# Optimization experiments

Measured on AMD Instinct MI355X. Metric: run time of the kernel, lower is better.

Reference implementation:

```python
import jax, jax.numpy as jnp
import numpy as np

B, N, C, CP, H, NQ, NK = 1, 2048, 128, 16, 8, 32, 128
DH = C // H
PAD = NK // 2 - NQ // 2  # 48
NB = N // NQ  # 64 windows


def _ln(x, gamma=None, beta=None, eps=1e-5):
    mu = jnp.mean(x, axis=-1, keepdims=True)
    var = jnp.var(x, axis=-1, keepdims=True)
    y = (x - mu) * jax.lax.rsqrt(var + eps)
    if gamma is not None:
        y = y * gamma
    if beta is not None:
        y = y + beta
    return y


def _forward(atom_single_repr, atom_single_proj, atom_pair_repr,
             gamma_s, Wg_ada, bg_ada, W_skip,
             gamma_p, beta_p, W_pair,
             Wq, Wk, Wv, Wg, bg, Wo, bo, W_out, b_out):
    # --- AdaLN(a, s): LN(a) modulated by s ---
    a_ln = _ln(atom_single_repr)                       # no affine
    s_ln = _ln(atom_single_proj, gamma_s)              # scale only
    a = jax.nn.sigmoid(s_ln @ Wg_ada + bg_ada) * a_ln + s_ln @ W_skip  # (B,N,C)

    # --- pair bias: LN + no-bias linear to heads ---
    pair_bias = _ln(atom_pair_repr, gamma_p, beta_p) @ W_pair          # (B,N,N,H)

    # --- extract_local_biases: pad key dim with -10000, take sliding blocks ---
    pb = jnp.pad(pair_bias, ((0, 0), (0, 0), (PAD, PAD), (0, 0)),
                 constant_values=-10000.0)                              # (B,N,N+2P,H)
    rows = pb.reshape(B, NB, NQ, N + 2 * PAD, H)
    col_idx = (jnp.arange(NB) * NQ)[:, None] + jnp.arange(NK)[None, :]  # (NB,NK)
    local_bias = jnp.take_along_axis(rows, col_idx[None, :, None, :, None], axis=3)
    bias = jnp.transpose(local_bias, (0, 1, 4, 2, 3))                   # (B,NB,H,NQ,NK)

    # --- partition_tensor for queries (stride==size, no pad) and keys/values ---
    q_x = a.reshape(B, NB, NQ, C)
    a_pad = jnp.pad(a, ((0, 0), (PAD, PAD), (0, 0)))
    kv_x = a_pad[:, col_idx, :]                                         # (B,NB,NK,C)

    # --- OpenFold-style gated attention per window ---
    q = (q_x @ Wq).reshape(B, NB, NQ, H, DH) * (DH ** -0.5)
    k = (kv_x @ Wk).reshape(B, NB, NK, H, DH)
    v = (kv_x @ Wv).reshape(B, NB, NK, H, DH)
    logits = jnp.einsum('bwqhd,bwkhd->bwhqk', q, k) + bias
    attn = jax.nn.softmax(logits, axis=-1)
    o = jnp.einsum('bwhqk,bwkhd->bwqhd', attn, v).reshape(B, NB, NQ, C)
    g = jax.nn.sigmoid(q_x @ Wg + bg)
    o = (o * g) @ Wo + bo                                               # (B,NB,NQ,C)
    out = o.reshape(B, N, C)

    # --- output gating ---
    return jax.nn.sigmoid(out @ W_out + b_out) * out


def setup_inputs() -> dict:
    key = jax.random.key(0)
    ks = jax.random.split(key, 16)
    s = 0.02
    return {
        'atom_single_repr': jax.random.normal(ks[0], (B, N, C), jnp.float32),
        'atom_single_proj': jax.random.normal(ks[1], (B, N, C), jnp.float32),
        'atom_pair_repr': jax.random.normal(ks[2], (B, N, N, CP), jnp.float32),
        'gamma_s': jnp.ones((C,), jnp.float32),
        'Wg_ada': s * jax.random.normal(ks[3], (C, C), jnp.float32),
        'bg_ada': jnp.zeros((C,), jnp.float32),
        'W_skip': s * jax.random.normal(ks[4], (C, C), jnp.float32),
        'gamma_p': jnp.ones((CP,), jnp.float32),
        'beta_p': jnp.zeros((CP,), jnp.float32),
        'W_pair': s * jax.random.normal(ks[5], (CP, H), jnp.float32),
        'Wq': s * jax.random.normal(ks[6], (C, C), jnp.float32),
        'Wk': s * jax.random.normal(ks[7], (C, C), jnp.float32),
        'Wv': s * jax.random.normal(ks[8], (C, C), jnp.float32),
        'Wg': s * jax.random.normal(ks[9], (C, C), jnp.float32),
        'bg': jnp.ones((C,), jnp.float32),
        'Wo': s * jax.random.normal(ks[10], (C, C), jnp.float32),
        'bo': jnp.zeros((C,), jnp.float32),
        'W_out': s * jax.random.normal(ks[11], (C, C), jnp.float32),
        'b_out': -2.0 * jnp.ones((C,), jnp.float32),
    }


def reference(atom_single_repr, atom_single_proj, atom_pair_repr,
              gamma_s, Wg_ada, bg_ada, W_skip, gamma_p, beta_p, W_pair,
              Wq, Wk, Wv, Wg, bg, Wo, bo, W_out, b_out):
    return _forward(atom_single_repr, atom_single_proj, atom_pair_repr,
                    gamma_s, Wg_ada, bg_ada, W_skip, gamma_p, beta_p, W_pair,
                    Wq, Wk, Wv, Wg, bg, Wo, bo, W_out, b_out)
```

## Files before the change

kernel.cpp:

```cpp
#include <hip/hip_runtime.h>
#include <math.h>

#define NTOK 2048
#define CC   128
#define CPP  16
#define HH   8
#define DHH  16
#define NQW  32
#define NKW  128
#define PADW 48
#define NBW  64

__device__ __forceinline__ float sigm(float x) { return 1.0f / (1.0f + expf(-x)); }

__global__ __launch_bounds__(512) void k1_fused(
    const float* __restrict__ x1, const float* __restrict__ x2,
    const float* __restrict__ gamma_s,
    const float* __restrict__ Wg_ada, const float* __restrict__ bg_ada,
    const float* __restrict__ W_skip,
    const float* __restrict__ Wq, const float* __restrict__ Wk,
    const float* __restrict__ Wv, const float* __restrict__ Wg,
    const float* __restrict__ bg,
    const float* __restrict__ pair,
    const float* __restrict__ gamma_p, const float* __restrict__ beta_p,
    const float* __restrict__ W_pair,
    float* __restrict__ qb, float* __restrict__ kb,
    float* __restrict__ vb, float* __restrict__ gb,
    float* __restrict__ bias)
{
  const int b   = blockIdx.x;
  const int tid = threadIdx.x;

  if (b < 256) {
    __shared__ float sln[8][132];
    __shared__ float aln[8][132];
    __shared__ float as_[8][132];
    const int r0 = b * 8;

    {
      const int r = tid >> 6, t = tid & 63, c0 = t * 2;
      const int row = r0 + r;
      float2 v1 = *(const float2*)(x1 + (size_t)row * CC + c0);
      float2 v2 = *(const float2*)(x2 + (size_t)row * CC + c0);
      float s1 = v1.x + v1.y, p1 = v1.x * v1.x + v1.y * v1.y;
      float s2 = v2.x + v2.y, p2 = v2.x * v2.x + v2.y * v2.y;
#pragma unroll
      for (int m = 1; m < 64; m <<= 1) {
        s1 += __shfl_xor(s1, m); p1 += __shfl_xor(p1, m);
        s2 += __shfl_xor(s2, m); p2 += __shfl_xor(p2, m);
      }
      const float rc = 1.0f / 128.0f;
      float mu1 = s1 * rc, mu2 = s2 * rc;
      float rs1 = rsqrtf(p1 * rc - mu1 * mu1 + 1e-5f);
      float rs2 = rsqrtf(p2 * rc - mu2 * mu2 + 1e-5f);
      float2 gs = *(const float2*)(gamma_s + c0);
      aln[r][c0]     = (v1.x - mu1) * rs1;
      aln[r][c0 + 1] = (v1.y - mu1) * rs1;
      sln[r][c0]     = (v2.x - mu2) * rs2 * gs.x;
      sln[r][c0 + 1] = (v2.y - mu2) * rs2 * gs.y;
    }
    __syncthreads();

    {
      const int rh = tid >> 7, cg = tid & 127;
      const int ra = rh * 2, rb = rh * 2 + 1;
      float g0 = 0.f, g1 = 0.f, s0 = 0.f, s1 = 0.f;
#pragma unroll 4
      for (int k4 = 0; k4 < 32; ++k4) {
        float4 a0 = *(const float4*)(&sln[ra][k4 * 4]);
        float4 a1 = *(const float4*)(&sln[rb][k4 * 4]);
#define S1STEP(AX, J) { \
        float wg = Wg_ada[(k4 * 4 + J) * CC + cg]; \
        float wk = W_skip[(k4 * 4 + J) * CC + cg]; \
        g0 = fmaf(a0.AX, wg, g0); g1 = fmaf(a1.AX, wg, g1); \
        s0 = fmaf(a0.AX, wk, s0); s1 = fmaf(a1.AX, wk, s1); }
        S1STEP(x, 0) S1STEP(y, 1) S1STEP(z, 2) S1STEP(w, 3)
#undef S1STEP
      }
      float bga = bg_ada[cg];
      as_[ra][cg] = sigm(g0 + bga) * aln[ra][cg] + s0;
      as_[rb][cg] = sigm(g1 + bga) * aln[rb][cg] + s1;
    }
    __syncthreads();

    {
      const int wv  = tid >> 6;
      const int m   = wv & 3;
      const int rh2 = wv >> 2;
      const int l   = tid & 63;
      const int c0  = l * 2;
      const int rb0 = rh2 * 4;
      const float* Wm = (m == 0) ? Wq : (m == 1) ? Wk : (m == 2) ? Wv : Wg;
      float2 c0_ = {0.f, 0.f}, c1_ = {0.f, 0.f}, c2_ = {0.f, 0.f}, c3_ = {0.f, 0.f};
#pragma unroll 4
      for (int k4 = 0; k4 < 32; ++k4) {
        float4 ra0 = *(const float4*)(&as_[rb0 + 0][k4 * 4]);
        float4 ra1 = *(const float4*)(&as_[rb0 + 1][k4 * 4]);
        float4 ra2 = *(const float4*)(&as_[rb0 + 2][k4 * 4]);
        float4 ra3 = *(const float4*)(&as_[rb0 + 3][k4 * 4]);
#define PJSTEP(AX, J) { \
        float2 wv2 = *(const float2*)(Wm + (k4 * 4 + J) * CC + c0); \
        c0_.x = fmaf(ra0.AX, wv2.x, c0_.x); c0_.y = fmaf(ra0.AX, wv2.y, c0_.y); \
        c1_.x = fmaf(ra1.AX, wv2.x, c1_.x); c1_.y = fmaf(ra1.AX, wv2.y, c1_.y); \
        c2_.x = fmaf(ra2.AX, wv2.x, c2_.x); c2_.y = fmaf(ra2.AX, wv2.y, c2_.y); \
        c3_.x = fmaf(ra3.AX, wv2.x, c3_.x); c3_.y = fmaf(ra3.AX, wv2.y, c3_.y); }
        PJSTEP(x, 0) PJSTEP(y, 1) PJSTEP(z, 2) PJSTEP(w, 3)
#undef PJSTEP
      }
      if (m == 0) {
#define QST(I, CI) { float2 r; r.x = CI.x * 0.25f; r.y = CI.y * 0.25f; \
        *(float2*)(qb + (size_t)(r0 + rb0 + I) * CC + c0) = r; }
        QST(0, c0_) QST(1, c1_) QST(2, c2_) QST(3, c3_)
#undef QST
      } else if (m == 1) {
#define KST(I, CI) *(float2*)(kb + (size_t)(r0 + rb0 + I) * CC + c0) = CI;
        KST(0, c0_) KST(1, c1_) KST(2, c2_) KST(3, c3_)
#undef KST
      } else if (m == 2) {
#define VST(I, CI) *(float2*)(vb + (size_t)(r0 + rb0 + I) * CC + c0) = CI;
        VST(0, c0_) VST(1, c1_) VST(2, c2_) VST(3, c3_)
#undef VST
      } else {
        float2 bgv = *(const float2*)(bg + c0);
#define GST(I, CI) { float2 r; r.x = sigm(CI.x + bgv.x); r.y = sigm(CI.y + bgv.y); \
        *(float2*)(gb + (size_t)(r0 + rb0 + I) * CC + c0) = r; }
        GST(0, c0_) GST(1, c1_) GST(2, c2_) GST(3, c3_)
#undef GST
      }
    }
  } else {
    __shared__ float wp[CPP * HH];
    __shared__ float gp[CPP];
    __shared__ float bp[CPP];
    if (tid < CPP * HH) wp[tid] = W_pair[tid];
    if (tid < CPP) { gp[tid] = gamma_p[tid]; bp[tid] = beta_p[tid]; }
    __syncthreads();

    const int i  = (b - 256) * 4 + (tid >> 7);
    const int w  = i >> 5;
    const int qq = i & 31;
    const int k  = tid & 127;
    const int j  = w * NQW + k - PADW;

    float bh[HH];
    if (j >= 0 && j < NTOK) {
      const float* p = pair + ((size_t)i * NTOK + j) * CPP;
      float x[CPP];
#pragma unroll
      for (int u4 = 0; u4 < CPP; u4 += 4) {
        float4 v = *(const float4*)(p + u4);
        x[u4] = v.x; x[u4 + 1] = v.y; x[u4 + 2] = v.z; x[u4 + 3] = v.w;
      }
      float s = 0.f;
#pragma unroll
      for (int c = 0; c < CPP; ++c) s += x[c];
      float mu = s * (1.0f / CPP);
      float vv = 0.f;
#pragma unroll
      for (int c = 0; c < CPP; ++c) { float d = x[c] - mu; vv = fmaf(d, d, vv); }
      float rs = rsqrtf(vv * (1.0f / CPP) + 1e-5f);
#pragma unroll
      for (int h = 0; h < HH; ++h) bh[h] = 0.f;
#pragma unroll
      for (int c = 0; c < CPP; ++c) {
        float y = (x[c] - mu) * rs * gp[c] + bp[c];
#pragma unroll
        for (int h = 0; h < HH; ++h) bh[h] = fmaf(y, wp[c * HH + h], bh[h]);
      }
    } else {
#pragma unroll
      for (int h = 0; h < HH; ++h) bh[h] = -10000.0f;
    }
#pragma unroll
    for (int h = 0; h < HH; ++h)
      bias[((size_t)((w * HH + h) * NQW + qq)) * NKW + k] = bh[h];
  }
}

__global__ __launch_bounds__(128) void attn_kernel(
    const float* __restrict__ qb, const float* __restrict__ kb,
    const float* __restrict__ vb, const float* __restrict__ bias,
    float* __restrict__ ob)
{
  __shared__ float qs[16][20];
  __shared__ float ks[NKW][20];
  __shared__ float vs[NKW][20];
  __shared__ float bs[16][132];
  const int u   = blockIdx.x;
  const int w   = u >> 4;
  const int h   = (u >> 1) & 7;
  const int qh  = u & 1;
  const int tid = threadIdx.x;

  if (tid < 64) {
    int qr = tid >> 2, c4 = (tid & 3) * 4;
    float4 v = *(const float4*)(qb + (size_t)(w * NQW + qh * 16 + qr) * CC + h * DHH + c4);
    *(float4*)(&qs[qr][c4]) = v;
  }
#pragma unroll
  for (int it = 0; it < 4; ++it) {
    int idx = tid + it * 128;
    int kr = idx >> 2, c4 = (idx & 3) * 4;
    int j = w * NQW + kr - PADW;
    float4 kv = make_float4(0.f, 0.f, 0.f, 0.f);
    float4 vv = make_float4(0.f, 0.f, 0.f, 0.f);
    if (j >= 0 && j < NTOK) {
      kv = *(const float4*)(kb + (size_t)j * CC + h * DHH + c4);
      vv = *(const float4*)(vb + (size_t)j * CC + h * DHH + c4);
    }
    *(float4*)(&ks[kr][c4]) = kv;
    *(float4*)(&vs[kr][c4]) = vv;
  }
  const float* bt = bias + (size_t)(w * HH + h) * NQW * NKW + (size_t)qh * 16 * NKW;
#pragma unroll
  for (int it = 0; it < 4; ++it) {
    int idx = tid + it * 128;
    int qr = idx >> 5, k4 = (idx & 31) * 4;
    float4 bv = *(const float4*)(bt + qr * NKW + k4);
    *(float4*)(&bs[qr][k4]) = bv;
  }
  __syncthreads();

  const int qg = tid >> 4;
  const int t  = tid & 15;
  const int r0 = qg * 2, r1 = r0 + 1;

  float4 qa0 = *(float4*)(&qs[r0][0]);
  float4 qa1 = *(float4*)(&qs[r0][4]);
  float4 qa2 = *(float4*)(&qs[r0][8]);
  float4 qa3 = *(float4*)(&qs[r0][12]);
  float4 qb0 = *(float4*)(&qs[r1][0]);
  float4 qb1 = *(float4*)(&qs[r1][4]);
  float4 qb2 = *(float4*)(&qs[r1][8]);
  float4 qb3 = *(float4*)(&qs[r1][12]);

  float l0[8], l1[8];
#pragma unroll
  for (int i = 0; i < 8; ++i) {
    int k = t + 16 * i;
    const float* kr = &ks[k][0];
    float4 k0 = *(const float4*)(kr);
    float4 k1 = *(const float4*)(kr + 4);
    float4 k2 = *(const float4*)(kr + 8);
    float4 k3 = *(const float4*)(kr + 12);
    float da = 0.f, db = 0.f;
    da = fmaf(qa0.x, k0.x, da); da = fmaf(qa0.y, k0.y, da);
    da = fmaf(qa0.z, k0.z, da); da = fmaf(qa0.w, k0.w, da);
    da = fmaf(qa1.x, k1.x, da); da = fmaf(qa1.y, k1.y, da);
    da = fmaf(qa1.z, k1.z, da); da = fmaf(qa1.w, k1.w, da);
    da = fmaf(qa2.x, k2.x, da); da = fmaf(qa2.y, k2.y, da);
    da = fmaf(qa2.z, k2.z, da); da = fmaf(qa2.w, k2.w, da);
    da = fmaf(qa3.x, k3.x, da); da = fmaf(qa3.y, k3.y, da);
    da = fmaf(qa3.z, k3.z, da); da = fmaf(qa3.w, k3.w, da);
    db = fmaf(qb0.x, k0.x, db); db = fmaf(qb0.y, k0.y, db);
    db = fmaf(qb0.z, k0.z, db); db = fmaf(qb0.w, k0.w, db);
    db = fmaf(qb1.x, k1.x, db); db = fmaf(qb1.y, k1.y, db);
    db = fmaf(qb1.z, k1.z, db); db = fmaf(qb1.w, k1.w, db);
    db = fmaf(qb2.x, k2.x, db); db = fmaf(qb2.y, k2.y, db);
    db = fmaf(qb2.z, k2.z, db); db = fmaf(qb2.w, k2.w, db);
    db = fmaf(qb3.x, k3.x, db); db = fmaf(qb3.y, k3.y, db);
    db = fmaf(qb3.z, k3.z, db); db = fmaf(qb3.w, k3.w, db);
    l0[i] = da + bs[r0][k];
    l1[i] = db + bs[r1][k];
  }

  float m0 = l0[0], m1 = l1[0];
#pragma unroll
  for (int i = 1; i < 8; ++i) { m0 = fmaxf(m0, l0[i]); m1 = fmaxf(m1, l1[i]); }
#pragma unroll
  for (int m = 1; m < 16; m <<= 1) {
    m0 = fmaxf(m0, __shfl_xor(m0, m));
    m1 = fmaxf(m1, __shfl_xor(m1, m));
  }
  float s0 = 0.f, s1 = 0.f;
  float p0[8], p1[8];
#pragma unroll
  for (int i = 0; i < 8; ++i) {
    p0[i] = expf(l0[i] - m0); s0 += p0[i];
    p1[i] = expf(l1[i] - m1); s1 += p1[i];
  }
#pragma unroll
  for (int m = 1; m < 16; m <<= 1) {
    s0 += __shfl_xor(s0, m);
    s1 += __shfl_xor(s1, m);
  }
  float inv0 = 1.0f / s0, inv1 = 1.0f / s1;
#pragma unroll
  for (int i = 0; i < 8; ++i) { p0[i] *= inv0; p1[i] *= inv1; }

  float o0[16], o1[16];
#pragma unroll
  for (int d = 0; d < 16; ++d) { o0[d] = 0.f; o1[d] = 0.f; }
#pragma unroll
  for (int i = 0; i < 8; ++i) {
    int k = t + 16 * i;
    const float* vr = &vs[k][0];
    float4 v0 = *(const float4*)(vr);
    float4 v1 = *(const float4*)(vr + 4);
    float4 v2 = *(const float4*)(vr + 8);
    float4 v3 = *(const float4*)(vr + 12);
    float pa = p0[i], pb = p1[i];
    o0[0]  = fmaf(pa, v0.x, o0[0]);  o0[1]  = fmaf(pa, v0.y, o0[1]);
    o0[2]  = fmaf(pa, v0.z, o0[2]);  o0[3]  = fmaf(pa, v0.w, o0[3]);
    o0[4]  = fmaf(pa, v1.x, o0[4]);  o0[5]  = fmaf(pa, v1.y, o0[5]);
    o0[6]  = fmaf(pa, v1.z, o0[6]);  o0[7]  = fmaf(pa, v1.w, o0[7]);
    o0[8]  = fmaf(pa, v2.x, o0[8]);  o0[9]  = fmaf(pa, v2.y, o0[9]);
    o0[10] = fmaf(pa, v2.z, o0[10]); o0[11] = fmaf(pa, v2.w, o0[11]);
    o0[12] = fmaf(pa, v3.x, o0[12]); o0[13] = fmaf(pa, v3.y, o0[13]);
    o0[14] = fmaf(pa, v3.z, o0[14]); o0[15] = fmaf(pa, v3.w, o0[15]);
    o1[0]  = fmaf(pb, v0.x, o1[0]);  o1[1]  = fmaf(pb, v0.y, o1[1]);
    o1[2]  = fmaf(pb, v0.z, o1[2]);  o1[3]  = fmaf(pb, v0.w, o1[3]);
    o1[4]  = fmaf(pb, v1.x, o1[4]);  o1[5]  = fmaf(pb, v1.y, o1[5]);
    o1[6]  = fmaf(pb, v1.z, o1[6]);  o1[7]  = fmaf(pb, v1.w, o1[7]);
    o1[8]  = fmaf(pb, v2.x, o1[8]);  o1[9]  = fmaf(pb, v2.y, o1[9]);
    o1[10] = fmaf(pb, v2.z, o1[10]); o1[11] = fmaf(pb, v2.w, o1[11]);
    o1[12] = fmaf(pb, v3.x, o1[12]); o1[13] = fmaf(pb, v3.y, o1[13]);
    o1[14] = fmaf(pb, v3.z, o1[14]); o1[15] = fmaf(pb, v3.w, o1[15]);
  }
#pragma unroll
  for (int d = 0; d < 16; ++d) {
#pragma unroll
    for (int m = 1; m < 16; m <<= 1) {
      o0[d] += __shfl_xor(o0[d], m);
      o1[d] += __shfl_xor(o1[d], m);
    }
  }
  float w0 = 0.f, w1 = 0.f;
#pragma unroll
  for (int d = 0; d < 16; ++d) {
    w0 = (t == d) ? o0[d] : w0;
    w1 = (t == d) ? o1[d] : w1;
  }
  ob[(size_t)(w * NQW + qh * 16 + r0) * CC + h * DHH + t] = w0;
  ob[(size_t)(w * NQW + qh * 16 + r1) * CC + h * DHH + t] = w1;
}

__global__ __launch_bounds__(256) void k3_out(
    const float* __restrict__ ob_, const float* __restrict__ gb_,
    const float* __restrict__ Wo, const float* __restrict__ bo,
    const float* __restrict__ W_out, const float* __restrict__ b_out,
    float* __restrict__ out)
{
  __shared__ float og[4][132];
  __shared__ float us[4][132];
  const int r0  = blockIdx.x * 4;
  const int tid = threadIdx.x;
  {
    const int r = tid >> 6, t = tid & 63, c0 = t * 2;
    float2 o2 = *(const float2*)(ob_ + (size_t)(r0 + r) * CC + c0);
    float2 g2 = *(const float2*)(gb_ + (size_t)(r0 + r) * CC + c0);
    og[r][c0]     = o2.x * g2.x;
    og[r][c0 + 1] = o2.y * g2.y;
  }
  __syncthreads();

  const int rg = tid >> 7;
  const int cg = tid & 127;
  const int ra = rg * 2, rb = rg * 2 + 1;

  float u0 = 0.f, u1 = 0.f;
#pragma unroll 4
  for (int k4 = 0; k4 < 32; ++k4) {
    float4 a0 = *(const float4*)(&og[ra][k4 * 4]);
    float4 a1 = *(const float4*)(&og[rb][k4 * 4]);
#define O1STEP(AX, J) { \
    float wv = Wo[(k4 * 4 + J) * CC + cg]; \
    u0 = fmaf(a0.AX, wv, u0); u1 = fmaf(a1.AX, wv, u1); }
    O1STEP(x, 0) O1STEP(y, 1) O1STEP(z, 2) O1STEP(w, 3)
#undef O1STEP
  }
  float bov = bo[cg];
  u0 += bov; u1 += bov;
  us[ra][cg] = u0;
  us[rb][cg] = u1;
  __syncthreads();

  float a0s = 0.f, a1s = 0.f;
#pragma unroll 4
  for (int k4 = 0; k4 < 32; ++k4) {
    float4 a0 = *(const float4*)(&us[ra][k4 * 4]);
    float4 a1 = *(const float4*)(&us[rb][k4 * 4]);
#define O2STEP(AX, J) { \
    float wv = W_out[(k4 * 4 + J) * CC + cg]; \
    a0s = fmaf(a0.AX, wv, a0s); a1s = fmaf(a1.AX, wv, a1s); }
    O2STEP(x, 0) O2STEP(y, 1) O2STEP(z, 2) O2STEP(w, 3)
#undef O2STEP
  }
  float b2 = b_out[cg];
  out[(size_t)(r0 + ra) * CC + cg] = sigm(a0s + b2) * u0;
  out[(size_t)(r0 + rb) * CC + cg] = sigm(a1s + b2) * u1;
}

extern "C" void kernel_launch(void* const* d_in, const int* in_sizes, int n_in,
                              void* d_out, int out_size, void* d_ws, size_t ws_size,
                              hipStream_t stream) {
  (void)in_sizes; (void)n_in; (void)out_size; (void)ws_size;
  const float* x1      = (const float*)d_in[0];
  const float* x2      = (const float*)d_in[1];
  const float* pair    = (const float*)d_in[2];
  const float* gamma_s = (const float*)d_in[3];
  const float* Wg_ada  = (const float*)d_in[4];
  const float* bg_ada  = (const float*)d_in[5];
  const float* W_skip  = (const float*)d_in[6];
  const float* gamma_p = (const float*)d_in[7];
  const float* beta_p  = (const float*)d_in[8];
  const float* W_pair  = (const float*)d_in[9];
  const float* Wq      = (const float*)d_in[10];
  const float* Wk      = (const float*)d_in[11];
  const float* Wv      = (const float*)d_in[12];
  const float* Wg      = (const float*)d_in[13];
  const float* bg      = (const float*)d_in[14];
  const float* Wo      = (const float*)d_in[15];
  const float* bo      = (const float*)d_in[16];
  const float* W_out   = (const float*)d_in[17];
  const float* b_out   = (const float*)d_in[18];

  float* ws   = (float*)d_ws;
  const size_t NC = (size_t)NTOK * CC;
  float* qb   = ws;
  float* kb   = ws + NC;
  float* vb   = ws + 2 * NC;
  float* gb   = ws + 3 * NC;
  float* obuf = ws + 4 * NC;
  float* bias = ws + 5 * NC;

  k1_fused<<<768, 512, 0, stream>>>(x1, x2, gamma_s, Wg_ada, bg_ada, W_skip,
                                    Wq, Wk, Wv, Wg, bg,
                                    pair, gamma_p, beta_p, W_pair,
                                    qb, kb, vb, gb, bias);
  attn_kernel<<<1024, 128, 0, stream>>>(qb, kb, vb, bias, obuf);
  k3_out<<<512, 256, 0, stream>>>(obuf, gb, Wo, bo, W_out, b_out,
                                  (float*)d_out);
}
```

Baseline: 44.39 us.

## Fuse windowed attention into output projection kernel

Merges the attention kernel and the output projection kernel so each block computes attention for 4 query rows across all heads (two heads per iteration), then gates and projects in shared memory. This removes one kernel launch and the global round trip of the attention output buffer. In exchange each window's K/V is reloaded by 8 blocks covering all heads, multiplying K/V read traffic. Heads are also processed sequentially with extra barriers.

New measurement: 50.26 us. 1.13x slower.

```diff
diff --git a/kernel.cpp b/kernel.cpp
--- a/kernel.cpp
+++ b/kernel.cpp
@@ -177,180 +177,148 @@
   }
 }
 
-__global__ __launch_bounds__(128) void attn_kernel(
+__global__ __launch_bounds__(256) void attn_out_kernel(
     const float* __restrict__ qb, const float* __restrict__ kb,
-    const float* __restrict__ vb, const float* __restrict__ bias,
-    float* __restrict__ ob)
-{
-  __shared__ float qs[16][20];
-  __shared__ float ks[NKW][20];
-  __shared__ float vs[NKW][20];
-  __shared__ float bs[16][132];
-  const int u   = blockIdx.x;
-  const int w   = u >> 4;
-  const int h   = (u >> 1) & 7;
-  const int qh  = u & 1;
-  const int tid = threadIdx.x;
-
-  if (tid < 64) {
-    int qr = tid >> 2, c4 = (tid & 3) * 4;
-    float4 v = *(const float4*)(qb + (size_t)(w * NQW + qh * 16 + qr) * CC + h * DHH + c4);
-    *(float4*)(&qs[qr][c4]) = v;
-  }
-#pragma unroll
-  for (int it = 0; it < 4; ++it) {
-    int idx = tid + it * 128;
-    int kr = idx >> 2, c4 = (idx & 3) * 4;
-    int j = w * NQW + kr - PADW;
-    float4 kv = make_float4(0.f, 0.f, 0.f, 0.f);
-    float4 vv = make_float4(0.f, 0.f, 0.f, 0.f);
-    if (j >= 0 && j < NTOK) {
-      kv = *(const float4*)(kb + (size_t)j * CC + h * DHH + c4);
-      vv = *(const float4*)(vb + (size_t)j * CC + h * DHH + c4);
-    }
-    *(float4*)(&ks[kr][c4]) = kv;
-    *(float4*)(&vs[kr][c4]) = vv;
-  }
-  const float* bt = bias + (size_t)(w * HH + h) * NQW * NKW + (size_t)qh * 16 * NKW;
-#pragma unroll
-  for (int it = 0; it < 4; ++it) {
-    int idx = tid + it * 128;
-    int qr = idx >> 5, k4 = (idx & 31) * 4;
-    float4 bv = *(const float4*)(bt + qr * NKW + k4);
-    *(float4*)(&bs[qr][k4]) = bv;
-  }
-  __syncthreads();
-
-  const int qg = tid >> 4;
-  const int t  = tid & 15;
-  const int r0 = qg * 2, r1 = r0 + 1;
-
-  float4 qa0 = *(float4*)(&qs[r0][0]);
-  float4 qa1 = *(float4*)(&qs[r0][4]);
-  float4 qa2 = *(float4*)(&qs[r0][8]);
-  float4 qa3 = *(float4*)(&qs[r0][12]);
-  float4 qb0 = *(float4*)(&qs[r1][0]);
-  float4 qb1 = *(float4*)(&qs[r1][4]);
-  float4 qb2 = *(float4*)(&qs[r1][8]);
-  float4 qb3 = *(float4*)(&qs[r1][12]);
-
-  float l0[8], l1[8];
-#pragma unroll
-  for (int i = 0; i < 8; ++i) {
-    int k = t + 16 * i;
-    const float* kr = &ks[k][0];
-    float4 k0 = *(const float4*)(kr);
-    float4 k1 = *(const float4*)(kr + 4);
-    float4 k2 = *(const float4*)(kr + 8);
-    float4 k3 = *(const float4*)(kr + 12);
-    float da = 0.f, db = 0.f;
-    da = fmaf(qa0.x, k0.x, da); da = fmaf(qa0.y, k0.y, da);
-    da = fmaf(qa0.z, k0.z, da); da = fmaf(qa0.w, k0.w, da);
-    da = fmaf(qa1.x, k1.x, da); da = fmaf(qa1.y, k1.y, da);
-    da = fmaf(qa1.z, k1.z, da); da = fmaf(qa1.w, k1.w, da);
-    da = fmaf(qa2.x, k2.x, da); da = fmaf(qa2.y, k2.y, da);
-    da = fmaf(qa2.z, k2.z, da); da = fmaf(qa2.w, k2.w, da);
-    da = fmaf(qa3.x, k3.x, da); da = fmaf(qa3.y, k3.y, da);
-    da = fmaf(qa3.z, k3.z, da); da = fmaf(qa3.w, k3.w, da);
-    db = fmaf(qb0.x, k0.x, db); db = fmaf(qb0.y, k0.y, db);
-    db = fmaf(qb0.z, k0.z, db); db = fmaf(qb0.w, k0.w, db);
-    db = fmaf(qb1.x, k1.x, db); db = fmaf(qb1.y, k1.y, db);
-    db = fmaf(qb1.z, k1.z, db); db = fmaf(qb1.w, k1.w, db);
-    db = fmaf(qb2.x, k2.x, db); db = fmaf(qb2.y, k2.y, db);
-    db = fmaf(qb2.z, k2.z, db); db = fmaf(qb2.w, k2.w, db);
-    db = fmaf(qb3.x, k3.x, db); db = fmaf(qb3.y, k3.y, db);
-    db = fmaf(qb3.z, k3.z, db); db = fmaf(qb3.w, k3.w, db);
-    l0[i] = da + bs[r0][k];
-    l1[i] = db + bs[r1][k];
-  }
-
-  float m0 = l0[0], m1 = l1[0];
-#pragma unroll
-  for (int i = 1; i < 8; ++i) { m0 = fmaxf(m0, l0[i]); m1 = fmaxf(m1, l1[i]); }
-#pragma unroll
-  for (int m = 1; m < 16; m <<= 1) {
-    m0 = fmaxf(m0, __shfl_xor(m0, m));
-    m1 = fmaxf(m1, __shfl_xor(m1, m));
-  }
-  float s0 = 0.f, s1 = 0.f;
-  float p0[8], p1[8];
-#pragma unroll
-  for (int i = 0; i < 8; ++i) {
-    p0[i] = expf(l0[i] - m0); s0 += p0[i];
-    p1[i] = expf(l1[i] - m1); s1 += p1[i];
-  }
-#pragma unroll
-  for (int m = 1; m < 16; m <<= 1) {
-    s0 += __shfl_xor(s0, m);
-    s1 += __shfl_xor(s1, m);
-  }
-  float inv0 = 1.0f / s0, inv1 = 1.0f / s1;
-#pragma unroll
-  for (int i = 0; i < 8; ++i) { p0[i] *= inv0; p1[i] *= inv1; }
-
-  float o0[16], o1[16];
-#pragma unroll
-  for (int d = 0; d < 16; ++d) { o0[d] = 0.f; o1[d] = 0.f; }
-#pragma unroll
-  for (int i = 0; i < 8; ++i) {
-    int k = t + 16 * i;
-    const float* vr = &vs[k][0];
-    float4 v0 = *(const float4*)(vr);
-    float4 v1 = *(const float4*)(vr + 4);
-    float4 v2 = *(const float4*)(vr + 8);
-    float4 v3 = *(const float4*)(vr + 12);
-    float pa = p0[i], pb = p1[i];
-    o0[0]  = fmaf(pa, v0.x, o0[0]);  o0[1]  = fmaf(pa, v0.y, o0[1]);
-    o0[2]  = fmaf(pa, v0.z, o0[2]);  o0[3]  = fmaf(pa, v0.w, o0[3]);
-    o0[4]  = fmaf(pa, v1.x, o0[4]);  o0[5]  = fmaf(pa, v1.y, o0[5]);
-    o0[6]  = fmaf(pa, v1.z, o0[6]);  o0[7]  = fmaf(pa, v1.w, o0[7]);
-    o0[8]  = fmaf(pa, v2.x, o0[8]);  o0[9]  = fmaf(pa, v2.y, o0[9]);
-    o0[10] = fmaf(pa, v2.z, o0[10]); o0[11] = fmaf(pa, v2.w, o0[11]);
-    o0[12] = fmaf(pa, v3.x, o0[12]); o0[13] = fmaf(pa, v3.y, o0[13]);
-    o0[14] = fmaf(pa, v3.z, o0[14]); o0[15] = fmaf(pa, v3.w, o0[15]);
-    o1[0]  = fmaf(pb, v0.x, o1[0]);  o1[1]  = fmaf(pb, v0.y, o1[1]);
-    o1[2]  = fmaf(pb, v0.z, o1[2]);  o1[3]  = fmaf(pb, v0.w, o1[3]);
-    o1[4]  = fmaf(pb, v1.x, o1[4]);  o1[5]  = fmaf(pb, v1.y, o1[5]);
-    o1[6]  = fmaf(pb, v1.z, o1[6]);  o1[7]  = fmaf(pb, v1.w, o1[7]);
-    o1[8]  = fmaf(pb, v2.x, o1[8]);  o1[9]  = fmaf(pb, v2.y, o1[9]);
-    o1[10] = fmaf(pb, v2.z, o1[10]); o1[11] = fmaf(pb, v2.w, o1[11]);
-    o1[12] = fmaf(pb, v3.x, o1[12]); o1[13] = fmaf(pb, v3.y, o1[13]);
-    o1[14] = fmaf(pb, v3.z, o1[14]); o1[15] = fmaf(pb, v3.w, o1[15]);
-  }
-#pragma unroll
-  for (int d = 0; d < 16; ++d) {
-#pragma unroll
-    for (int m = 1; m < 16; m <<= 1) {
-      o0[d] += __shfl_xor(o0[d], m);
-      o1[d] += __shfl_xor(o1[d], m);
-    }
-  }
-  float w0 = 0.f, w1 = 0.f;
-#pragma unroll
-  for (int d = 0; d < 16; ++d) {
-    w0 = (t == d) ? o0[d] : w0;
-    w1 = (t == d) ? o1[d] : w1;
-  }
-  ob[(size_t)(w * NQW + qh * 16 + r0) * CC + h * DHH + t] = w0;
-  ob[(size_t)(w * NQW + qh * 16 + r1) * CC + h * DHH + t] = w1;
-}
-
-__global__ __launch_bounds__(256) void k3_out(
-    const float* __restrict__ ob_, const float* __restrict__ gb_,
+    const float* __restrict__ vb, const float* __restrict__ gb,
+    const float* __restrict__ bias,
     const float* __restrict__ Wo, const float* __restrict__ bo,
     const float* __restrict__ W_out, const float* __restrict__ b_out,
     float* __restrict__ out)
 {
+  __shared__ float qs[4][132];
+  __shared__ float ks[2][NKW][20];
+  __shared__ float vs[2][NKW][20];
+  __shared__ float bs[2][4][132];
+  __shared__ float oacc[4][132];
   __shared__ float og[4][132];
   __shared__ float us[4][132];
-  const int r0  = blockIdx.x * 4;
+
+  const int b   = blockIdx.x;
+  const int w   = b >> 3;
+  const int q4  = b & 7;
+  const int r0  = w * NQW + q4 * 4;
   const int tid = threadIdx.x;
+
   {
-    const int r = tid >> 6, t = tid & 63, c0 = t * 2;
-    float2 o2 = *(const float2*)(ob_ + (size_t)(r0 + r) * CC + c0);
-    float2 g2 = *(const float2*)(gb_ + (size_t)(r0 + r) * CC + c0);
-    og[r][c0]     = o2.x * g2.x;
-    og[r][c0 + 1] = o2.y * g2.y;
+    const int r = tid >> 6, c0 = (tid & 63) * 2;
+    float2 qv = *(const float2*)(qb + (size_t)(r0 + r) * CC + c0);
+    qs[r][c0]     = qv.x;
+    qs[r][c0 + 1] = qv.y;
+  }
+
+#pragma unroll 1
+  for (int it = 0; it < 4; ++it) {
+    __syncthreads();
+
+#pragma unroll
+    for (int s = 0; s < 4; ++s) {
+      int u   = tid + s * 256;
+      int hh  = u >> 9;
+      int rem = u & 511;
+      int kr  = rem >> 2, c4 = (rem & 3) * 4;
+      int j   = w * NQW + kr - PADW;
+      float4 kv = make_float4(0.f, 0.f, 0.f, 0.f);
+      float4 vv = make_float4(0.f, 0.f, 0.f, 0.f);
+      if (j >= 0 && j < NTOK) {
+        kv = *(const float4*)(kb + (size_t)j * CC + (it * 2 + hh) * DHH + c4);
+        vv = *(const float4*)(vb + (size_t)j * CC + (it * 2 + hh) * DHH + c4);
+      }
+      *(float4*)(&ks[hh][kr][c4]) = kv;
+      *(float4*)(&vs[hh][kr][c4]) = vv;
+    }
+    {
+      int hh  = tid >> 7;
+      int rem = tid & 127;
+      int qr  = rem >> 5, k4 = (rem & 31) * 4;
+      float4 bv = *(const float4*)(bias +
+          ((size_t)((w * HH + it * 2 + hh) * NQW + q4 * 4 + qr)) * NKW + k4);
+      *(float4*)(&bs[hh][qr][k4]) = bv;
+    }
+    __syncthreads();
+
+    const int hp = tid >> 7;
+    const int t7 = tid & 127;
+    const int qr = t7 >> 5;
+    const int t  = t7 & 31;
+    const int h  = it * 2 + hp;
+
+    float4 q0 = *(float4*)(&qs[qr][h * DHH + 0]);
+    float4 q1 = *(float4*)(&qs[qr][h * DHH + 4]);
+    float4 q2 = *(float4*)(&qs[qr][h * DHH + 8]);
+    float4 q3 = *(float4*)(&qs[qr][h * DHH + 12]);
+
+    float l[4];
+#pragma unroll
+    for (int i = 0; i < 4; ++i) {
+      int k = t + 32 * i;
+      const float* kr_ = &ks[hp][k][0];
+      float4 k0 = *(const float4*)(kr_);
+      float4 k1 = *(const float4*)(kr_ + 4);
+      float4 k2 = *(const float4*)(kr_ + 8);
+      float4 k3 = *(const float4*)(kr_ + 12);
+      float d = 0.f;
+      d = fmaf(q0.x, k0.x, d); d = fmaf(q0.y, k0.y, d);
+      d = fmaf(q0.z, k0.z, d); d = fmaf(q0.w, k0.w, d);
+      d = fmaf(q1.x, k1.x, d); d = fmaf(q1.y, k1.y, d);
+      d = fmaf(q1.z, k1.z, d); d = fmaf(q1.w, k1.w, d);
+      d = fmaf(q2.x, k2.x, d); d = fmaf(q2.y, k2.y, d);
+      d = fmaf(q2.z, k2.z, d); d = fmaf(q2.w, k2.w, d);
+      d = fmaf(q3.x, k3.x, d); d = fmaf(q3.y, k3.y, d);
+      d = fmaf(q3.z, k3.z, d); d = fmaf(q3.w, k3.w, d);
+      l[i] = d + bs[hp][qr][k];
+    }
+
+    float m0 = fmaxf(fmaxf(l[0], l[1]), fmaxf(l[2], l[3]));
+#pragma unroll
+    for (int m = 1; m < 32; m <<= 1) m0 = fmaxf(m0, __shfl_xor(m0, m));
+    float p[4];
+    float s = 0.f;
+#pragma unroll
+    for (int i = 0; i < 4; ++i) { p[i] = expf(l[i] - m0); s += p[i]; }
+#pragma unroll
+    for (int m = 1; m < 32; m <<= 1) s += __shfl_xor(s, m);
+    float inv = 1.0f / s;
+#pragma unroll
+    for (int i = 0; i < 4; ++i) p[i] *= inv;
+
+    float o16[16];
+#pragma unroll
+    for (int d = 0; d < 16; ++d) o16[d] = 0.f;
+#pragma unroll
+    for (int i = 0; i < 4; ++i) {
+      int k = t + 32 * i;
+      const float* vr = &vs[hp][k][0];
+      float4 v0 = *(const float4*)(vr);
+      float4 v1 = *(const float4*)(vr + 4);
+      float4 v2 = *(const float4*)(vr + 8);
+      float4 v3 = *(const float4*)(vr + 12);
+      float pa = p[i];
+      o16[0]  = fmaf(pa, v0.x, o16[0]);  o16[1]  = fmaf(pa, v0.y, o16[1]);
+      o16[2]  = fmaf(pa, v0.z, o16[2]);  o16[3]  = fmaf(pa, v0.w, o16[3]);
+      o16[4]  = fmaf(pa, v1.x, o16[4]);  o16[5]  = fmaf(pa, v1.y, o16[5]);
+      o16[6]  = fmaf(pa, v1.z, o16[6]);  o16[7]  = fmaf(pa, v1.w, o16[7]);
+      o16[8]  = fmaf(pa, v2.x, o16[8]);  o16[9]  = fmaf(pa, v2.y, o16[9]);
+      o16[10] = fmaf(pa, v2.z, o16[10]); o16[11] = fmaf(pa, v2.w, o16[11]);
+      o16[12] = fmaf(pa, v3.x, o16[12]); o16[13] = fmaf(pa, v3.y, o16[13]);
+      o16[14] = fmaf(pa, v3.z, o16[14]); o16[15] = fmaf(pa, v3.w, o16[15]);
+    }
+#pragma unroll
+    for (int d = 0; d < 16; ++d) {
+#pragma unroll
+      for (int m = 1; m < 32; m <<= 1) o16[d] += __shfl_xor(o16[d], m);
+    }
+    float wsel = 0.f;
+#pragma unroll
+    for (int d = 0; d < 16; ++d) wsel = (t == d) ? o16[d] : wsel;
+    if (t < 16) oacc[qr][h * DHH + t] = wsel;
+  }
+  __syncthreads();
+
+  {
+    const int r = tid >> 6, c0 = (tid & 63) * 2;
+    float2 g2 = *(const float2*)(gb + (size_t)(r0 + r) * CC + c0);
+    og[r][c0]     = oacc[r][c0]     * g2.x;
+    og[r][c0 + 1] = oacc[r][c0 + 1] * g2.y;
   }
   __syncthreads();
 
@@ -421,14 +389,13 @@
   float* kb   = ws + NC;
   float* vb   = ws + 2 * NC;
   float* gb   = ws + 3 * NC;
-  float* obuf = ws + 4 * NC;
-  float* bias = ws + 5 * NC;
+  float* bias = ws + 4 * NC;
 
   k1_fused<<<768, 512, 0, stream>>>(x1, x2, gamma_s, Wg_ada, bg_ada, W_skip,
                                     Wq, Wk, Wv, Wg, bg,
                                     pair, gamma_p, beta_p, W_pair,
                                     qb, kb, vb, gb, bias);
-  attn_kernel<<<1024, 128, 0, stream>>>(qb, kb, vb, bias, obuf);
-  k3_out<<<512, 256, 0, stream>>>(obuf, gb, Wo, bo, W_out, b_out,
-                                  (float*)d_out);
+  attn_out_kernel<<<512, 256, 0, stream>>>(qb, kb, vb, gb, bias,
+                                           Wo, bo, W_out, b_out,
+                                           (float*)d_out);
 }
```
